# Performance work log

Measured on AMD Instinct MI355X. Metric: run time of the kernel, lower is better.

## Reference

```python
import jax, jax.numpy as jnp
import numpy as np

# Problem sizes (match input_specs)
B, D, N, M, C = 2, 128, 131072, 131072, 128
IGNORE = -1  # config.data.ignore_label


def setup_inputs() -> dict:
    key = jax.random.key(0)
    k1, k2, k3, k4, k5 = jax.random.split(key, 5)
    vb = jax.random.randint(k1, (N, 1), 0, B)
    vxyz = jax.random.randint(k2, (N, 3), 0, D)
    coords = jnp.concatenate([vb, vxyz], axis=1).astype(jnp.int32)  # (N,4) [b,x,y,z]
    qb = jax.random.randint(k3, (M, 1), 0, B).astype(jnp.float32)
    qxyz = jax.random.uniform(k4, (M, 3), minval=0.0, maxval=float(D - 1))
    query_points = jnp.concatenate([qb, qxyz], axis=1)  # (M,4) [b,x,y,z]
    features = jax.random.normal(k5, (N, C), dtype=jnp.float32)  # (N,C)
    return {"coords": coords, "features": features, "query_points": query_points}


def reference(coords, features, query_points):
    n_vox = coords.shape[0]
    b = coords[:, 0]
    xyz = coords[:, 1:]
    # per-batch coordinate shift (torch.amin per batch), scale_factor == 1
    shift = jax.ops.segment_min(xyz, b, num_segments=B)  # (B,3)
    xyz = xyz - shift[b]
    qb = query_points[:, 0].astype(jnp.int32)
    q = query_points[:, 1:] - shift[qb].astype(query_points.dtype)  # (M,3)

    # dense occupancy: voxel index at occupied cells, IGNORE elsewhere
    occ = jnp.full((B, D, D, D), IGNORE, dtype=jnp.int32)
    occ = occ.at[b, xyz[:, 0], xyz[:, 1], xyz[:, 2]].set(
        jnp.arange(n_vox, dtype=jnp.int32))

    # 8-corner trilinear gather
    q0 = jnp.floor(q)
    f = q - q0                              # fractional part, (M,3)
    q0i = q0.astype(jnp.int32)
    offs = jnp.array([[i, j, k] for i in (0, 1) for j in (0, 1) for k in (0, 1)],
                     dtype=jnp.int32)       # (8,3)
    corner = q0i[:, None, :] + offs[None]   # (M,8,3)
    inb = jnp.all((corner >= 0) & (corner < D), axis=-1)  # (M,8)
    cc = jnp.clip(corner, 0, D - 1)
    idx = occ[qb[:, None], cc[..., 0], cc[..., 1], cc[..., 2]]  # (M,8)

    # trilinear weights: prod over dims of f (corner==1) or 1-f (corner==0)
    w = jnp.prod(jnp.where(offs[None].astype(bool), f[:, None, :], 1.0 - f[:, None, :]),
                 axis=-1)                   # (M,8)
    valid = inb & (idx >= 0)
    wv = jnp.where(valid, w, 0.0)
    wsum = wv.sum(-1)                       # (M,)

    safe_idx = jnp.clip(idx, 0, None)
    gathered = features[safe_idx]           # (M,8,C)
    query_features = jnp.einsum('mk,mkc->mc', wv, gathered) / \
        jnp.maximum(wsum, 1e-8)[:, None]    # normalized by valid weight mass

    interpolation_indices = jnp.where(valid, idx, IGNORE)
    accum_voxel_weights = jax.ops.segment_sum(
        wv.reshape(-1), safe_idx.reshape(-1), num_segments=n_vox)
    return query_features, interpolation_indices, wv, accum_voxel_weights
```

## Files before the change

kernel.cpp:

```cpp
#include <hip/hip_runtime.h>
#include <limits.h>

#define DIM 128
#define NVOX 131072
#define NQ 131072
#define NCELL (2 * DIM * DIM * DIM)
#define BITWORDS (NCELL / 64)

#define QF_OFF  0
#define IDX_OFF (NQ * 128)
#define WV_OFF  (IDX_OFF + NQ * 8)
#define ACC_OFF (WV_OFF + NQ * 8)

#define SHIFT_BLOCKS 64

typedef float vf2 __attribute__((ext_vector_type(2)));

#define WREDUCE_MIN(mv)                                       \
    _Pragma("unroll")                                         \
    for (int off = 32; off >= 1; off >>= 1)                   \
        mv = min(mv, __shfl_xor(mv, off, 64));

__device__ __forceinline__ int cell_of(int b, int x, int y, int z) {
    return (b << 21) + (x << 14) + (y << 7) + z;
}

__global__ __launch_bounds__(256) void k_prep(const int* __restrict__ coords,
                                              int* __restrict__ sp,
                                              unsigned long long* __restrict__ bitmap,
                                              int* __restrict__ idxg,
                                              float* __restrict__ accum) {
    int tid = blockIdx.x * 256 + threadIdx.x;
    int4 c = ((const int4*)coords)[tid];
    idxg[cell_of(c.x, c.y, c.z, c.w)] = -1;
    if (tid < BITWORDS) bitmap[tid] = 0ull;
    accum[tid] = 0.f;

    if (blockIdx.x < SHIFT_BLOCKS) {
        __shared__ int sm[4][6];
        int i0 = blockIdx.x * 256 + threadIdx.x;
        int sstride = SHIFT_BLOCKS * 256;
        int m0 = INT_MAX, m1 = INT_MAX, m2 = INT_MAX;
        int m3 = INT_MAX, m4 = INT_MAX, m5 = INT_MAX;
        const int4* c4 = (const int4*)coords;
        for (int i = i0; i < NVOX; i += sstride) {
            int4 v = c4[i];
            if (v.x == 0) { m0 = min(m0, v.y); m1 = min(m1, v.z); m2 = min(m2, v.w); }
            else          { m3 = min(m3, v.y); m4 = min(m4, v.z); m5 = min(m5, v.w); }
        }
        WREDUCE_MIN(m0) WREDUCE_MIN(m1) WREDUCE_MIN(m2)
        WREDUCE_MIN(m3) WREDUCE_MIN(m4) WREDUCE_MIN(m5)
        int wave = threadIdx.x >> 6;
        if ((threadIdx.x & 63) == 0) {
            sm[wave][0] = m0; sm[wave][1] = m1; sm[wave][2] = m2;
            sm[wave][3] = m3; sm[wave][4] = m4; sm[wave][5] = m5;
        }
        __syncthreads();
        if (threadIdx.x == 0) {
            #pragma unroll
            for (int k = 0; k < 6; ++k)
                sp[k * SHIFT_BLOCKS + blockIdx.x] =
                    min(min(sm[0][k], sm[1][k]), min(sm[2][k], sm[3][k]));
        }
    }
}

__global__ __launch_bounds__(256) void k_build(const int* __restrict__ coords,
                                               unsigned long long* __restrict__ bitmap,
                                               int* __restrict__ idxg) {
    int i = blockIdx.x * 256 + threadIdx.x;
    int4 c = ((const int4*)coords)[i];
    int cell = cell_of(c.x, c.y, c.z, c.w);
    atomicOr(&bitmap[cell >> 6], 1ull << (cell & 63));
    atomicMax(&idxg[cell], i);
}

__device__ __forceinline__ void load_shift(const int* __restrict__ sp, int* sh) {
    if (threadIdx.x < 64) {
        int l = threadIdx.x;
        #pragma unroll
        for (int k = 0; k < 6; ++k) {
            int v = sp[k * SHIFT_BLOCKS + l];
            WREDUCE_MIN(v)
            if (l == 0) sh[k] = v;
        }
    }
}

__global__ __launch_bounds__(256) void k_query(
    const float* __restrict__ qpts, const float* __restrict__ feats,
    const unsigned long long* __restrict__ bitmap, const int* __restrict__ idxg,
    const int* __restrict__ sp, float* __restrict__ out) {
    __shared__ int sh[6];
    __shared__ int2  s_iw[256 * 8];
    __shared__ uint2 s_mi[256];
    load_shift(sp, sh);
    __syncthreads();

    int t = threadIdx.x;
    int q = blockIdx.x * 256 + t;

    float4 qp = ((const float4*)qpts)[q];
    int qb = (int)qp.x;
    int shx = sh[qb * 3 + 0], shy = sh[qb * 3 + 1], shz = sh[qb * 3 + 2];
    float fx0 = floorf(qp.y), fy0 = floorf(qp.z), fz0 = floorf(qp.w);
    float fx = qp.y - fx0, fy = qp.z - fy0, fz = qp.w - fz0;
    int ix = (int)fx0, iy = (int)fy0, iz = (int)fz0;

    int cells[8]; bool okc[8]; float wc[8];
#pragma unroll
    for (int k = 0; k < 8; ++k) {
        const int ox = (k >> 2) & 1, oy = (k >> 1) & 1, oz = k & 1;
        int ux = ix + ox, uy = iy + oy, uz = iz + oz;
        okc[k] = ((unsigned)(ux - shx) < DIM) && ((unsigned)(uy - shy) < DIM) &&
                 ((unsigned)(uz - shz) < DIM) &&
                 ((unsigned)ux < DIM) && ((unsigned)uy < DIM) && ((unsigned)uz < DIM);
        int cx = min(max(ux, 0), DIM - 1);
        int cy = min(max(uy, 0), DIM - 1);
        int cz = min(max(uz, 0), DIM - 1);
        cells[k] = cell_of(qb, cx, cy, cz);
        wc[k] = (ox ? fx : 1.f - fx) * (oy ? fy : 1.f - fy) * (oz ? fz : 1.f - fz);
    }
    unsigned long long wb[8];
#pragma unroll
    for (int k = 0; k < 8; ++k) wb[k] = bitmap[cells[k] >> 6];
    bool val[8];
#pragma unroll
    for (int k = 0; k < 8; ++k)
        val[k] = okc[k] && (((wb[k] >> (cells[k] & 63)) & 1ull) != 0ull);
    int idxk[8];
#pragma unroll
    for (int k = 0; k < 8; ++k) idxk[k] = val[k] ? idxg[cells[k]] : -1;

    float wsum = 0.f; unsigned msk = 0u;
#pragma unroll
    for (int k = 0; k < 8; ++k) {
        float wv = val[k] ? wc[k] : 0.f;
        wsum += wv;
        if (wv != 0.f) {
            msk |= 1u << k;
            atomicAdd(out + ACC_OFF + idxk[k], wv);
        }
        s_iw[t * 8 + k] = make_int2(idxk[k], __float_as_int(wv));
    }
    float inv = __builtin_amdgcn_rcpf(fmaxf(wsum, 1e-8f));
    s_mi[t] = make_uint2(msk, __float_as_uint(inv));
    __syncthreads();

    size_t sbase = (size_t)blockIdx.x * 2048;
#pragma unroll
    for (int j = 0; j < 8; ++j) {
        int2 iw = s_iw[j * 256 + t];
        __builtin_nontemporal_store((float)iw.x, out + IDX_OFF + sbase + j * 256 + t);
        __builtin_nontemporal_store(__int_as_float(iw.y), out + WV_OFF + sbase + j * 256 + t);
    }

    int lane = t & 63;
    int wq0 = (t >> 6) * 64;
    const vf2* f2 = (const vf2*)feats;
    vf2* qf = (vf2*)(out + QF_OFF);
    size_t qgbase = (size_t)blockIdx.x * 256;
    for (int g = 0; g < 64; ++g) {
        int qq = wq0 + g;
        uint2 mi = s_mi[qq];
        unsigned m = __builtin_amdgcn_readfirstlane(mi.x);
        vf2 acc = (vf2){0.f, 0.f};
        while (m) {
            int j = __ffs(m) - 1; m &= m - 1;
            int2 iw = s_iw[qq * 8 + j];
            int row = __builtin_amdgcn_readfirstlane(iw.x);
            float wv = __int_as_float(iw.y);
            vf2 fv = f2[(size_t)row * 64 + lane];
            acc.x = fmaf(wv, fv.x, acc.x);
            acc.y = fmaf(wv, fv.y, acc.y);
        }
        float iv = __uint_as_float(mi.y);
        vf2 r;
        r.x = acc.x * iv;
        r.y = acc.y * iv;
        __builtin_nontemporal_store(r, qf + (qgbase + qq) * 64 + lane);
    }
}

extern "C" void kernel_launch(void* const* d_in, const int* in_sizes, int n_in,
                              void* d_out, int out_size, void* d_ws, size_t ws_size,
                              hipStream_t stream) {
    const int*   coords = (const int*)d_in[0];
    const float* feats  = (const float*)d_in[1];
    const float* qpts   = (const float*)d_in[2];
    float* out = (float*)d_out;

    int* sp = (int*)d_ws;
    unsigned long long* bitmap = (unsigned long long*)((char*)d_ws + 4096);
    int* idxg = (int*)((char*)d_ws + 4096 + BITWORDS * 8);

    k_prep<<<NVOX / 256, 256, 0, stream>>>(coords, sp, bitmap, idxg, out + ACC_OFF);
    k_build<<<NVOX / 256, 256, 0, stream>>>(coords, bitmap, idxg);
    k_query<<<NQ / 256, 256, 0, stream>>>(qpts, feats, bitmap, idxg, sp, out);
}
```

Baseline: 45.53 us.

## Split query kernel into probe and gather kernels with finer wave granularity

Splits the fused query kernel in two. A probe kernel computes corner indices and weights, writes them with vectorized per-query stores, and saves the mask and inverse weight sum to workspace. A separate gather kernel then reads these back from global memory and accumulates feature rows, with each wave handling 16 queries instead of 64, which gives more blocks for better load balance and occupancy. The cost is an extra kernel launch plus a round trip of the index and weight data through global memory, and the nontemporal stores become regular stores.

```diff
diff --git a/kernel.cpp b/kernel.cpp
--- a/kernel.cpp
+++ b/kernel.cpp
@@ -85,17 +85,16 @@
             if (l == 0) sh[k] = v;
         }
     }
-}
-
-__global__ __launch_bounds__(256) void k_query(
-    const float* __restrict__ qpts, const float* __restrict__ feats,
+    __syncthreads();
+}
+
+__global__ __launch_bounds__(256) void k_probe(
+    const float* __restrict__ qpts,
     const unsigned long long* __restrict__ bitmap, const int* __restrict__ idxg,
-    const int* __restrict__ sp, float* __restrict__ out) {
+    const int* __restrict__ sp, uint2* __restrict__ mi_out,
+    float* __restrict__ out) {
     __shared__ int sh[6];
-    __shared__ int2  s_iw[256 * 8];
-    __shared__ uint2 s_mi[256];
     load_shift(sp, sh);
-    __syncthreads();
 
     int t = threadIdx.x;
     int q = blockIdx.x * 256 + t;
@@ -132,44 +131,54 @@
 #pragma unroll
     for (int k = 0; k < 8; ++k) idxk[k] = val[k] ? idxg[cells[k]] : -1;
 
+    float idxf[8], wvf[8];
     float wsum = 0.f; unsigned msk = 0u;
 #pragma unroll
     for (int k = 0; k < 8; ++k) {
         float wv = val[k] ? wc[k] : 0.f;
         wsum += wv;
+        idxf[k] = (float)idxk[k];
+        wvf[k] = wv;
         if (wv != 0.f) {
             msk |= 1u << k;
             atomicAdd(out + ACC_OFF + idxk[k], wv);
         }
-        s_iw[t * 8 + k] = make_int2(idxk[k], __float_as_int(wv));
     }
     float inv = __builtin_amdgcn_rcpf(fmaxf(wsum, 1e-8f));
-    s_mi[t] = make_uint2(msk, __float_as_uint(inv));
-    __syncthreads();
-
-    size_t sbase = (size_t)blockIdx.x * 2048;
-#pragma unroll
-    for (int j = 0; j < 8; ++j) {
-        int2 iw = s_iw[j * 256 + t];
-        __builtin_nontemporal_store((float)iw.x, out + IDX_OFF + sbase + j * 256 + t);
-        __builtin_nontemporal_store(__int_as_float(iw.y), out + WV_OFF + sbase + j * 256 + t);
-    }
-
-    int lane = t & 63;
-    int wq0 = (t >> 6) * 64;
+    mi_out[q] = make_uint2(msk, __float_as_uint(inv));
+
+    float4* oi = (float4*)(out + IDX_OFF + (size_t)q * 8);
+    float4* ow = (float4*)(out + WV_OFF + (size_t)q * 8);
+    oi[0] = make_float4(idxf[0], idxf[1], idxf[2], idxf[3]);
+    oi[1] = make_float4(idxf[4], idxf[5], idxf[6], idxf[7]);
+    ow[0] = make_float4(wvf[0], wvf[1], wvf[2], wvf[3]);
+    ow[1] = make_float4(wvf[4], wvf[5], wvf[6], wvf[7]);
+}
+
+#define QPW 16
+__global__ __launch_bounds__(256) void k_gather(
+    const float* __restrict__ feats, const uint2* __restrict__ mi_in,
+    float* __restrict__ out) {
+    int lane = threadIdx.x & 63;
+    int gwave = blockIdx.x * 4 + (threadIdx.x >> 6);
+    int qbase = gwave * QPW;
+
     const vf2* f2 = (const vf2*)feats;
     vf2* qf = (vf2*)(out + QF_OFF);
-    size_t qgbase = (size_t)blockIdx.x * 256;
-    for (int g = 0; g < 64; ++g) {
-        int qq = wq0 + g;
-        uint2 mi = s_mi[qq];
+    const float* oidx = out + IDX_OFF;
+    const float* owv  = out + WV_OFF;
+
+#pragma unroll
+    for (int g = 0; g < QPW; ++g) {
+        int q = qbase + g;
+        uint2 mi = mi_in[q];
         unsigned m = __builtin_amdgcn_readfirstlane(mi.x);
         vf2 acc = (vf2){0.f, 0.f};
         while (m) {
             int j = __ffs(m) - 1; m &= m - 1;
-            int2 iw = s_iw[qq * 8 + j];
-            int row = __builtin_amdgcn_readfirstlane(iw.x);
-            float wv = __int_as_float(iw.y);
+            float idxf = oidx[q * 8 + j];
+            float wv   = owv[q * 8 + j];
+            int row = (int)__builtin_amdgcn_readfirstlane(idxf);
             vf2 fv = f2[(size_t)row * 64 + lane];
             acc.x = fmaf(wv, fv.x, acc.x);
             acc.y = fmaf(wv, fv.y, acc.y);
@@ -178,7 +187,7 @@
         vf2 r;
         r.x = acc.x * iv;
         r.y = acc.y * iv;
-        __builtin_nontemporal_store(r, qf + (qgbase + qq) * 64 + lane);
+        qf[(size_t)q * 64 + lane] = r;
     }
 }
 
@@ -192,9 +201,11 @@
 
     int* sp = (int*)d_ws;
     unsigned long long* bitmap = (unsigned long long*)((char*)d_ws + 4096);
-    int* idxg = (int*)((char*)d_ws + 4096 + BITWORDS * 8);
+    int*   idxg = (int*)((char*)d_ws + 4096 + BITWORDS * 8);
+    uint2* mi   = (uint2*)((char*)d_ws + 4096 + BITWORDS * 8 + (size_t)NCELL * 4);
 
     k_prep<<<NVOX / 256, 256, 0, stream>>>(coords, sp, bitmap, idxg, out + ACC_OFF);
     k_build<<<NVOX / 256, 256, 0, stream>>>(coords, bitmap, idxg);
-    k_query<<<NQ / 256, 256, 0, stream>>>(qpts, feats, bitmap, idxg, sp, out);
-}
+    k_probe<<<NQ / 256, 256, 0, stream>>>(qpts, bitmap, idxg, sp, mi, out);
+    k_gather<<<NQ / (QPW * 4), 256, 0, stream>>>(feats, mi, out);
+}
```

Measured after the change: 49.38 us. 8.5% more time.
